# Kernel optimization log

Measured on AMD Instinct MI355X. Metric: run time of the kernel, lower is better.

## Reference

```python
import jax, jax.numpy as jnp
import numpy as np

B, T, IN, HID, BR, OUT = 128, 250, 700, 1024, 4, 20
VTH1, VTH2, DT = 0.5, 0.5, 1.0

# heaviside spike with multi-gaussian surrogate grad (DH-SNN ActFun_adp)
@jax.custom_vjp
def spike_fn(v):
    return (v > 0).astype(v.dtype)

def _spike_fwd(v):
    return spike_fn(v), v

def _spike_bwd(v, g):
    gamma, lens, scale, hight = 0.5, 0.5, 6.0, 0.15
    def gauss(x, mu, sigma):
        return jnp.exp(-((x - mu) ** 2) / (2.0 * sigma ** 2)) / (jnp.sqrt(2.0 * jnp.pi) * sigma)
    sg = (gauss(v, 0.0, lens) * (1.0 + hight)
          - gauss(v, lens, scale * lens) * hight
          - gauss(v, -lens, scale * lens) * hight)
    return (g * sg * gamma,)

spike_fn.defvjp(_spike_fwd, _spike_bwd)

def _make_mask(rng):
    # each output neuron's BR branches see disjoint equal slices of a random permutation
    K = IN + HID  # pad == 0 since (IN+HID) % BR == 0
    seg = K // BR
    mask = np.zeros((HID * BR, K), dtype=np.int32)
    for i in range(HID):
        seq = rng.permutation(K)
        for j in range(BR):
            mask[i * BR + j, seq[j * seg:(j + 1) * seg]] = 1
    return mask

def setup_inputs() -> dict:
    key = jax.random.key(0)
    ks = jax.random.split(key, 10)
    K = IN + HID
    x = jax.random.uniform(ks[0], (B, T, IN), dtype=jnp.float32)
    W1 = jax.random.normal(ks[1], (HID * BR, K), dtype=jnp.float32) / jnp.sqrt(jnp.float32(K))
    b1 = jnp.zeros((HID * BR,), jnp.float32)
    tau_m1 = jax.random.uniform(ks[2], (HID,), jnp.float32, 0.0, 4.0)
    tau_n = jax.random.uniform(ks[3], (HID, BR), jnp.float32, 0.0, 4.0)
    W2 = jax.random.normal(ks[4], (OUT, HID), dtype=jnp.float32) / jnp.sqrt(jnp.float32(HID))
    b2 = jnp.zeros((OUT,), jnp.float32)
    tau_m2 = jax.random.uniform(ks[5], (OUT,), jnp.float32, 0.0, 4.0)
    mem1_0 = jax.random.uniform(ks[6], (B, HID), jnp.float32)
    mem2_0 = jax.random.uniform(ks[7], (B, OUT), jnp.float32)
    mask = jnp.asarray(_make_mask(np.random.default_rng(0)))
    return dict(x=x, W1=W1, b1=b1, tau_m1=tau_m1, tau_n=tau_n, W2=W2, b2=b2,
                tau_m2=tau_m2, mem1_0=mem1_0, mem2_0=mem2_0, mask=mask)

def reference(x, W1, b1, tau_m1, tau_n, W2, b2, tau_m2, mem1_0, mem2_0, mask):
    bsz = x.shape[0]
    W1m = W1 * mask.astype(W1.dtype)  # branch-sparse dendritic weights
    alpha1 = jax.nn.sigmoid(tau_m1)   # [HID]
    beta = jax.nn.sigmoid(tau_n)      # [HID, BR]
    alpha2 = jax.nn.sigmoid(tau_m2)   # [OUT]
    spk1_0 = jnp.zeros((bsz, HID), x.dtype)
    d0 = jnp.zeros((bsz, HID, BR), x.dtype)
    spk2_0 = jnp.zeros((bsz, OUT), x.dtype)

    def step(carry, x_t):
        mem1, spk1, d_inp, mem2, spk2 = carry
        k_in = jnp.concatenate([x_t, spk1], axis=1)          # [B, IN+HID]
        ff = (k_in @ W1m.T + b1).reshape(bsz, HID, BR)       # dendritic branch input
        d_inp = beta * d_inp + (1.0 - beta) * ff             # per-branch decay
        l_in = d_inp.sum(axis=2)                             # [B, HID]
        mem1 = mem1 * alpha1 + (1.0 - alpha1) * l_in - VTH1 * spk1 * DT
        spk1 = spike_fn(mem1 - VTH1)
        d2 = spk1 @ W2.T + b2
        mem2 = mem2 * alpha2 + (1.0 - alpha2) * d2 - VTH2 * spk2 * DT
        spk2 = spike_fn(mem2 - VTH2)
        out = jax.nn.log_softmax(mem2, axis=1)
        return (mem1, spk1, d_inp, mem2, spk2), out

    _, ys = jax.lax.scan(step, (mem1_0, spk1_0, d0, mem2_0, spk2_0), jnp.swapaxes(x, 0, 1))
    return jnp.transpose(ys, (1, 2, 0))  # [B, OUT, T]
```

## Files before the change

### kernel.cpp

```cpp
#include <hip/hip_runtime.h>
#include <stdint.h>

#define BATCH 128
#define TSTEPS 250
#define NIN 700
#define NHID 1024
#define NBR 4
#define NOUT 20
#define KDIM 1724
#define NR 4096
#define VTH 0.5f

typedef float f32x4 __attribute__((ext_vector_type(4)));
typedef short s16x8 __attribute__((ext_vector_type(8)));


__global__ void setup_small(const float* __restrict__ tau_m1, const float* __restrict__ tau_n,
                            const float* __restrict__ tau_m2, const float* __restrict__ W2,
                            float* __restrict__ alpha1, float* __restrict__ beta,
                            float* __restrict__ alpha2, float* __restrict__ W2T) {
    int i = blockIdx.x * blockDim.x + threadIdx.x;
    if (i < NHID)  alpha1[i] = 1.f / (1.f + expf(-tau_m1[i]));
    if (i < NR)    beta[i]   = 1.f / (1.f + expf(-tau_n[i]));
    if (i < 32)    alpha2[i] = (i < NOUT) ? 1.f / (1.f + expf(-tau_m2[i])) : 0.f;
    if (i < NHID * 32) {
        int j = i >> 5, o = i & 31;
        W2T[i] = (o < NOUT) ? W2[o * NHID + j] : 0.f;
    }
}

__device__ __forceinline__ uint16_t f2bf_rne(float x) {
    uint32_t u = __float_as_uint(x);
    return (uint16_t)((u + 0x7FFFu + ((u >> 16) & 1u)) >> 16);
}

__global__ void setup_weights(const float* __restrict__ W1, const int* __restrict__ mask,
                              float* __restrict__ W1xT, uint16_t* __restrict__ fragH,
                              uint16_t* __restrict__ fragL) {
    const int total1 = NIN * NR;
    const int total2 = 256 * 16384;
    for (int i = blockIdx.x * blockDim.x + threadIdx.x; i < total1 + total2;
         i += gridDim.x * blockDim.x) {
        if (i < total1) {
            int k = i >> 12, r = i & 4095;
            size_t src = (size_t)r * KDIM + k;
            W1xT[i] = W1[src] * (float)mask[src];
        } else {
            int j2 = i - total1;
            int j = j2 & 7, lane = (j2 >> 3) & 63, ks = (j2 >> 9) & 31, blk = j2 >> 14;
            int k = ks * 32 + ((lane >> 4) & 3) * 8 + j;
            int r = blk * 16 + (lane & 15);
            size_t src = (size_t)r * KDIM + NIN + k;
            float w = W1[src] * (float)mask[src];
            uint16_t hb = f2bf_rne(w);
            float hf = __uint_as_float((uint32_t)hb << 16);
            fragH[j2] = hb;
            fragL[j2] = f2bf_rne(w - hf);
        }
    }
}

__global__ void init_state(const float* __restrict__ mem1_0, const float* __restrict__ mem2_0,
                           float* __restrict__ mem1, float* __restrict__ mem2,
                           float* __restrict__ spk2, float* __restrict__ d_inp,
                           uint32_t* __restrict__ spkg, uint32_t* __restrict__ bar) {
    int i = blockIdx.x * blockDim.x + threadIdx.x;
    if (i < BATCH * NR) d_inp[i] = 0.f;
    if (i < BATCH * NHID) mem1[i] = mem1_0[i];
    if (i < BATCH * NOUT) { mem2[i] = mem2_0[i]; spk2[i] = 0.f; }
    if (i < 8192) spkg[i] = 0u;
    if (i < 2048) bar[i] = 0u;
}


#define GBM 128
#define GBN 128
#define GBK 16

__global__ __launch_bounds__(256) void ffx_gemm(const float* __restrict__ x,
                                                const float* __restrict__ W1xT,
                                                const float* __restrict__ b1,
                                                float* __restrict__ ffx, int t0) {
    __shared__ float As[GBK][GBM];
    __shared__ float Bs[GBK][GBN];
    int dt = blockIdx.x, bn = blockIdx.y;
    int tid = threadIdx.x;
    int tn = tid & 15, tm = tid >> 4;

    float acc[8][8];
#pragma unroll
    for (int i = 0; i < 8; ++i)
#pragma unroll
        for (int j = 0; j < 8; ++j) acc[i][j] = 0.f;

    int m_l = tid >> 1;
    const float* xrow = x + ((size_t)m_l * TSTEPS + t0 + dt) * NIN;
    int kh = (tid & 1) * 8;
    int kb = tid >> 4;
    int nb = (tid & 15) * 8;

    for (int k0 = 0; k0 < NIN; k0 += GBK) {
        float av[8];
#pragma unroll
        for (int u = 0; u < 8; ++u) {
            int k = k0 + kh + u;
            av[u] = (k < NIN) ? xrow[k] : 0.f;
        }
#pragma unroll
        for (int u = 0; u < 8; ++u) As[kh + u][m_l] = av[u];

        bool kok = (k0 + kb) < NIN;
        const float* bp = W1xT + (size_t)(k0 + kb) * NR + bn * GBN + nb;
        float bv[8];
#pragma unroll
        for (int u = 0; u < 8; ++u) bv[u] = kok ? bp[u] : 0.f;
#pragma unroll
        for (int u = 0; u < 8; ++u) Bs[kb][nb + u] = bv[u];

        __syncthreads();
#pragma unroll
        for (int kk = 0; kk < GBK; ++kk) {
            float a[8], b[8];
#pragma unroll
            for (int u = 0; u < 8; ++u) a[u] = As[kk][tm * 8 + u];
#pragma unroll
            for (int u = 0; u < 8; ++u) b[u] = Bs[kk][tn * 8 + u];
#pragma unroll
            for (int i = 0; i < 8; ++i)
#pragma unroll
                for (int j = 0; j < 8; ++j) acc[i][j] += a[i] * b[j];
        }
        __syncthreads();
    }

    float bias[8];
#pragma unroll
    for (int j = 0; j < 8; ++j) bias[j] = b1[bn * GBN + tn * 8 + j];
#pragma unroll
    for (int i = 0; i < 8; ++i) {
        int brow = tm * 8 + i;
        float* cp = ffx + ((size_t)dt * BATCH + brow) * NR + bn * GBN + tn * 8;
#pragma unroll
        for (int j = 0; j < 8; ++j) cp[j] = acc[i][j] + bias[j];
    }
}


__global__ __launch_bounds__(1024) void persist6(
    const float* __restrict__ alpha1, const float* __restrict__ beta,
    const float* __restrict__ alpha2, float* __restrict__ mem1,
    float* __restrict__ mem2, float* __restrict__ spk2,
    float* __restrict__ d_inp, const uint16_t* __restrict__ fragH_g,
    const uint16_t* __restrict__ fragL_g, const float* __restrict__ W2T,
    const float* __restrict__ ffx, const float* __restrict__ b2v,
    float* __restrict__ out, uint32_t* __restrict__ spkg,
    uint32_t* __restrict__ bar, int t0, int tc, int last, int epoch0) {
    __shared__ __align__(16) uint16_t lds_fh[16384];
    __shared__ __align__(16) uint16_t lds_fl[16384];
    __shared__ uint32_t lds_spk[4096];
    __shared__ uint32_t lds_mask[128 * 33];
    __shared__ float lds_part[2560];
    __shared__ float lds_part2[2560];

    const int blk = blockIdx.x;
    const int tid = threadIdx.x;
    const int l   = tid & 63;
    const int wv  = tid >> 6;

    {
        const float4* sH = (const float4*)(fragH_g + (size_t)blk * 16384);
        const float4* sL = (const float4*)(fragL_g + (size_t)blk * 16384);
        for (int i4 = tid; i4 < 2048; i4 += 1024) {
            ((float4*)lds_fh)[i4] = sH[i4];
            ((float4*)lds_fl)[i4] = sL[i4];
        }
    }

    const int mt = wv & 7;
    const int kh = wv >> 3;
    const int arow = mt * 16 + (l & 15);
    const int ksl = ((l >> 4) & 3) * 8;

    const int ub    = tid >> 3;
    const int unrn  = (tid >> 1) & 3;
    const int uhalf = tid & 1;
    const int nrn_g = (blk << 2) + unrn;
    const int rl0   = unrn * 4 + uhalf * 2;
    const int r_g0  = (blk << 4) + rl0;
    const float bet0 = beta[r_g0];
    const float bet1 = beta[r_g0 + 1];
    const float al   = alpha1[nrn_g];
    float di0 = d_inp[(size_t)ub * NR + r_g0];
    float di1 = d_inp[(size_t)ub * NR + r_g0 + 1];
    float mm  = mem1[ub * NHID + nrn_g];

    const int o2 = tid & 31;
    const int sub = tid >> 5;
    const bool l2blk = (blk < 16) && ((sub & 3) == 0);
    const int b2b = (blk << 3) + (sub >> 2);
    float m2 = 0.f, s2v = 0.f, a2 = 0.f, bo = 0.f;
    if (l2blk && o2 < NOUT) {
        a2 = alpha2[o2];
        bo = b2v[o2];
        m2 = mem2[b2b * NOUT + o2];
        s2v = spk2[b2b * NOUT + o2];
    }

    const int grpid = blk & 15;
    uint32_t* grpcnt = &bar[32 * (1 + grpid)];
    uint32_t* goword = &bar[32 * (17 + grpid)];
    const bool leader = (blk >= 240);

    const int iters = tc + (last ? 1 : 0);
    for (int it = 0; it < iters; ++it) {
        const int tt = t0 + it;

        float ff0 = 0.f, ff1 = 0.f;
        if (tt < TSTEPS) {
            const float2 fv = *(const float2*)(ffx + (size_t)it * (BATCH * NR)
                                               + (size_t)ub * NR + r_g0);
            ff0 = fv.x; ff1 = fv.y;
        }

        if (it > 0) {
            if (tid == 0) {
                uint32_t tgt = (uint32_t)(epoch0 + it);
                if (leader) {
                    while (__hip_atomic_load(&bar[0], __ATOMIC_ACQUIRE,
                                             __HIP_MEMORY_SCOPE_AGENT) < 16u * tgt)
                        __builtin_amdgcn_s_sleep(2);
                    __hip_atomic_store(goword, tgt, __ATOMIC_RELEASE,
                                       __HIP_MEMORY_SCOPE_AGENT);
                } else {
                    while (__hip_atomic_load(goword, __ATOMIC_RELAXED,
                                             __HIP_MEMORY_SCOPE_AGENT) < tgt)
                        __builtin_amdgcn_s_sleep(2);
                }
            }
            __syncthreads();
        }

        {
            const uint32_t* spg = spkg + (size_t)((tt + 1) & 1) * 4096;
#pragma unroll
            for (int k = 0; k < 4; ++k) {
                int idx = tid + (k << 10);
                lds_spk[idx ^ ((idx >> 7) & 31)] =
                    __hip_atomic_load(&spg[idx], __ATOMIC_RELAXED, __HIP_MEMORY_SCOPE_AGENT);
            }
        }
        __syncthreads();

        {
            const int w = tid & 31;
            const int bq = tid >> 5;
            const int g = bq >> 1;
            uint32_t sw[8];
#pragma unroll
            for (int m = 0; m < 8; ++m) {
                int raw = (w << 7) + (m << 4) + g;
                sw[m] = lds_spk[raw ^ (w & 31)];
            }
#pragma unroll
            for (int u = 0; u < 4; ++u) {
                const int b = (bq << 2) + u;
                const int j = ((bq & 1) << 2) + u;
                uint32_t word = 0;
#pragma unroll
                for (int m = 0; m < 8; ++m)
                    word |= ((sw[m] >> (j << 2)) & 0xFu) << (m << 2);
                lds_mask[b * 33 + w] = word;
            }
        }
        __syncthreads();

        if (tt < TSTEPS) {
            f32x4 acc = {0.f, 0.f, 0.f, 0.f};
            const int maskbase = arow * 33;
#pragma unroll 4
            for (int i = 0; i < 16; ++i) {
                const int ks = kh * 16 + i;
                uint32_t bits = (lds_mask[maskbase + ks] >> ksl) & 0xFFu;
                union { uint32_t u[4]; s16x8 v; } a;
                a.u[0] = ((bits & 1u)  ? 0x3F80u : 0u) | ((bits & 2u)   ? 0x3F800000u : 0u);
                a.u[1] = ((bits & 4u)  ? 0x3F80u : 0u) | ((bits & 8u)   ? 0x3F800000u : 0u);
                a.u[2] = ((bits & 16u) ? 0x3F80u : 0u) | ((bits & 32u)  ? 0x3F800000u : 0u);
                a.u[3] = ((bits & 64u) ? 0x3F80u : 0u) | ((bits & 128u) ? 0x3F800000u : 0u);
                const s16x8 bh = *(const s16x8*)&lds_fh[(ks * 64 + l) * 8];
                const s16x8 bl = *(const s16x8*)&lds_fl[(ks * 64 + l) * 8];
                acc = __builtin_amdgcn_mfma_f32_16x16x32_bf16(a.v, bh, acc, 0, 0, 0);
                acc = __builtin_amdgcn_mfma_f32_16x16x32_bf16(a.v, bl, acc, 0, 0, 0);
            }
            float* pp = (kh == 0 ? lds_part : lds_part2)
                        + ((mt * 16 + (l & 15)) * 20 + ((l >> 4) & 3) * 4);
            *(float4*)pp = *(float4*)&acc;
        }
        __syncthreads();

        if (tt < TSTEPS) {
            const int pb = ((ub >> 4) * 16 + rl0) * 20 + (ub & 15);
            float s0 = lds_part[pb]      + lds_part2[pb];
            float s1 = lds_part[pb + 20] + lds_part2[pb + 20];
            di0 = bet0 * di0 + (1.f - bet0) * (s0 + ff0);
            di1 = bet1 * di1 + (1.f - bet1) * (s1 + ff1);
            float t2 = di0 + di1;
            float lsum = t2 + __shfl_xor(t2, 1);
            float sp_prev = (float)((lds_mask[ub * 33 + (nrn_g >> 5)] >> (nrn_g & 31)) & 1u);
            float mn = mm * al + (1.f - al) * lsum - VTH * sp_prev;
            mm = mn;
            bool spk = (mn - VTH) > 0.f;
            unsigned long long bal = __ballot(spk && (uhalf == 0));
            if (l == 0) {
                uint32_t dw = 0;
#pragma unroll
                for (int j = 0; j < 8; ++j) {
                    uint32_t v = (uint32_t)(bal >> (j * 8)) & 0x55u;
                    uint32_t nib = (v & 1u) | ((v >> 1) & 2u) | ((v >> 2) & 4u) | ((v >> 3) & 8u);
                    dw |= nib << (4 * j);
                }
                uint32_t* spn = spkg + (size_t)(tt & 1) * 4096;
                __hip_atomic_store(&spn[(blk << 4) + wv], dw, __ATOMIC_RELAXED,
                                   __HIP_MEMORY_SCOPE_AGENT);
            }
        }

        __syncthreads();
        if (it + 1 < iters && tid == 0) {
            uint32_t e16 = 16u * (uint32_t)(epoch0 + it + 1);
            uint32_t old = __hip_atomic_fetch_add(grpcnt, 1u, __ATOMIC_RELEASE,
                                                  __HIP_MEMORY_SCOPE_AGENT);
            if (old == e16 - 1u)
                __hip_atomic_fetch_add(&bar[0], 1u, __ATOMIC_RELEASE,
                                       __HIP_MEMORY_SCOPE_AGENT);
        }

        if (tt > 0 && l2blk) {
            const uint32_t* mw = &lds_mask[b2b * 33];
            float d2 = bo;
            for (int w = 0; w < 32; ++w) {
                uint32_t bits = mw[w];
                while (bits) {
                    int p = __builtin_ctz(bits);
                    bits &= bits - 1;
                    d2 += W2T[(((w << 5) + p) << 5) + o2];
                }
            }
            float m2n = m2 * a2 + (1.f - a2) * d2 - VTH * s2v;
            m2 = m2n;
            s2v = ((m2n - VTH) > 0.f) ? 1.f : 0.f;
            float v = (o2 < NOUT) ? m2n : -3.4e38f;
#pragma unroll
            for (int off = 16; off >= 1; off >>= 1) v = fmaxf(v, __shfl_xor(v, off, 32));
            float e = (o2 < NOUT) ? expf(m2n - v) : 0.f;
            float s = e;
#pragma unroll
            for (int off = 16; off >= 1; off >>= 1) s += __shfl_xor(s, off, 32);
            if (o2 < NOUT) out[((size_t)b2b * NOUT + o2) * TSTEPS + (tt - 1)] = (m2n - v) - logf(s);
        }
    }

    d_inp[(size_t)ub * NR + r_g0]     = di0;
    d_inp[(size_t)ub * NR + r_g0 + 1] = di1;
    if (uhalf == 0) mem1[ub * NHID + nrn_g] = mm;
    if (l2blk && o2 < NOUT) {
        mem2[b2b * NOUT + o2] = m2;
        spk2[b2b * NOUT + o2] = s2v;
    }
}


extern "C" void kernel_launch(void* const* d_in, const int* in_sizes, int n_in,
                              void* d_out, int out_size, void* d_ws, size_t ws_size,
                              hipStream_t stream) {
    const float* x      = (const float*)d_in[0];
    const float* W1     = (const float*)d_in[1];
    const float* b1     = (const float*)d_in[2];
    const float* tau_m1 = (const float*)d_in[3];
    const float* tau_n  = (const float*)d_in[4];
    const float* W2     = (const float*)d_in[5];
    const float* b2     = (const float*)d_in[6];
    const float* tau_m2 = (const float*)d_in[7];
    const float* mem1_0 = (const float*)d_in[8];
    const float* mem2_0 = (const float*)d_in[9];
    const int*   mask   = (const int*)d_in[10];
    float* out = (float*)d_out;

    float* ws = (float*)d_ws;
    size_t F = 0;
    float* alpha1 = ws + F; F += 1024;
    float* beta   = ws + F; F += 4096;
    float* alpha2 = ws + F; F += 32;
    float* mem1   = ws + F; F += BATCH * NHID;
    float* mem2   = ws + F; F += BATCH * NOUT;
    float* spk2   = ws + F; F += BATCH * NOUT;
    float* d_inp  = ws + F; F += BATCH * NR;
    float* W1xT   = ws + F; F += (size_t)NIN * NR;
    uint16_t* fragH = (uint16_t*)(ws + F); F += (size_t)256 * 16384 / 2;
    uint16_t* fragL = (uint16_t*)(ws + F); F += (size_t)256 * 16384 / 2;
    float* W2T    = ws + F; F += NHID * 32;
    uint32_t* spkg = (uint32_t*)(ws + F); F += 8192;
    uint32_t* bar  = (uint32_t*)(ws + F); F += 2048;
    float* ffx = ws + F;

    size_t ws_f = ws_size / 4;
    size_t avail = (ws_f > F) ? (ws_f - F) : 0;
    size_t per_t = (size_t)BATCH * NR;
    int Tc = (int)(avail / per_t);
    if (Tc < 1) Tc = 1;
    if (Tc > TSTEPS) Tc = TSTEPS;

    hipLaunchKernelGGL(setup_small, dim3(128), dim3(256), 0, stream,
                       tau_m1, tau_n, tau_m2, W2, alpha1, beta, alpha2, W2T);
    hipLaunchKernelGGL(setup_weights, dim3(2048), dim3(256), 0, stream,
                       W1, mask, W1xT, fragH, fragL);
    hipLaunchKernelGGL(init_state, dim3(2048), dim3(256), 0, stream,
                       mem1_0, mem2_0, mem1, mem2, spk2, d_inp, spkg, bar);

    int chunk_start = 0;
    int barriers_done = 0;
    while (chunk_start < TSTEPS) {
        int tc = TSTEPS - chunk_start;
        if (tc > Tc) tc = Tc;
        int last = (chunk_start + tc >= TSTEPS) ? 1 : 0;

        hipLaunchKernelGGL(ffx_gemm, dim3(tc, 32), dim3(256), 0, stream,
                           x, W1xT, b1, ffx, chunk_start);
        hipLaunchKernelGGL(persist6, dim3(256), dim3(1024), 0, stream,
                           alpha1, beta, alpha2, mem1, mem2, spk2, d_inp, fragH, fragL,
                           W2T, ffx, b2, out, spkg, bar, chunk_start, tc, last, barriers_done);

        int iters = tc + (last ? 1 : 0);
        barriers_done += iters - 1;
        chunk_start += tc;
    }
}
```

Measured before the change: 6.728 ms.

## Publish spikes in transposed global layout via atomic OR, drop LDS repack

Each timestep's spike bits are now written straight into a batch-major bitmask in global memory, using per-lane atomic OR into a 4-deep ring buffer, with a slot two steps ahead zeroed each step. Readers load their mask words directly from global, so the per-step LDS staging, the transpose/repack pass and two block-wide barriers go away. The cost is many small global atomics per step, and the correctness of the ring clearing depends on the grid barrier ordering.

```diff
diff --git a/kernel.cpp b/kernel.cpp
--- a/kernel.cpp
+++ b/kernel.cpp
@@ -63,12 +63,12 @@
 __global__ void init_state(const float* __restrict__ mem1_0, const float* __restrict__ mem2_0,
                            float* __restrict__ mem1, float* __restrict__ mem2,
                            float* __restrict__ spk2, float* __restrict__ d_inp,
-                           uint32_t* __restrict__ spkg, uint32_t* __restrict__ bar) {
+                           uint32_t* __restrict__ spkT, uint32_t* __restrict__ bar) {
     int i = blockIdx.x * blockDim.x + threadIdx.x;
     if (i < BATCH * NR) d_inp[i] = 0.f;
     if (i < BATCH * NHID) mem1[i] = mem1_0[i];
     if (i < BATCH * NOUT) { mem2[i] = mem2_0[i]; spk2[i] = 0.f; }
-    if (i < 8192) spkg[i] = 0u;
+    if (i < 4 * 4096) spkT[i] = 0u;
     if (i < 2048) bar[i] = 0u;
 }
 
@@ -146,19 +146,17 @@
 }
 
 
-__global__ __launch_bounds__(1024) void persist6(
+__global__ __launch_bounds__(1024) void persist8(
     const float* __restrict__ alpha1, const float* __restrict__ beta,
     const float* __restrict__ alpha2, float* __restrict__ mem1,
     float* __restrict__ mem2, float* __restrict__ spk2,
     float* __restrict__ d_inp, const uint16_t* __restrict__ fragH_g,
     const uint16_t* __restrict__ fragL_g, const float* __restrict__ W2T,
     const float* __restrict__ ffx, const float* __restrict__ b2v,
-    float* __restrict__ out, uint32_t* __restrict__ spkg,
+    float* __restrict__ out, uint32_t* __restrict__ spkT,
     uint32_t* __restrict__ bar, int t0, int tc, int last, int epoch0) {
     __shared__ __align__(16) uint16_t lds_fh[16384];
     __shared__ __align__(16) uint16_t lds_fl[16384];
-    __shared__ uint32_t lds_spk[4096];
-    __shared__ uint32_t lds_mask[128 * 33];
     __shared__ float lds_part[2560];
     __shared__ float lds_part2[2560];
 
@@ -240,47 +238,22 @@
             __syncthreads();
         }
 
-        {
-            const uint32_t* spg = spkg + (size_t)((tt + 1) & 1) * 4096;
-#pragma unroll
-            for (int k = 0; k < 4; ++k) {
-                int idx = tid + (k << 10);
-                lds_spk[idx ^ ((idx >> 7) & 31)] =
-                    __hip_atomic_load(&spg[idx], __ATOMIC_RELAXED, __HIP_MEMORY_SCOPE_AGENT);
-            }
-        }
-        __syncthreads();
-
-        {
-            const int w = tid & 31;
-            const int bq = tid >> 5;
-            const int g = bq >> 1;
-            uint32_t sw[8];
-#pragma unroll
-            for (int m = 0; m < 8; ++m) {
-                int raw = (w << 7) + (m << 4) + g;
-                sw[m] = lds_spk[raw ^ (w & 31)];
-            }
-#pragma unroll
-            for (int u = 0; u < 4; ++u) {
-                const int b = (bq << 2) + u;
-                const int j = ((bq & 1) << 2) + u;
-                uint32_t word = 0;
-#pragma unroll
-                for (int m = 0; m < 8; ++m)
-                    word |= ((sw[m] >> (j << 2)) & 0xFu) << (m << 2);
-                lds_mask[b * 33 + w] = word;
-            }
-        }
-        __syncthreads();
-
+        const uint32_t* spc = spkT + (size_t)(tt & 3) * 4096;
+
+        uint32_t spw = 0;
         if (tt < TSTEPS) {
+            spw = __hip_atomic_load(&spc[ub * 32 + (nrn_g >> 5)], __ATOMIC_RELAXED,
+                                    __HIP_MEMORY_SCOPE_AGENT);
+            uint32_t mw[16];
+#pragma unroll
+            for (int i = 0; i < 16; ++i)
+                mw[i] = __hip_atomic_load(&spc[arow * 32 + kh * 16 + i], __ATOMIC_RELAXED,
+                                          __HIP_MEMORY_SCOPE_AGENT);
             f32x4 acc = {0.f, 0.f, 0.f, 0.f};
-            const int maskbase = arow * 33;
 #pragma unroll 4
             for (int i = 0; i < 16; ++i) {
                 const int ks = kh * 16 + i;
-                uint32_t bits = (lds_mask[maskbase + ks] >> ksl) & 0xFFu;
+                uint32_t bits = (mw[i] >> ksl) & 0xFFu;
                 union { uint32_t u[4]; s16x8 v; } a;
                 a.u[0] = ((bits & 1u)  ? 0x3F80u : 0u) | ((bits & 2u)   ? 0x3F800000u : 0u);
                 a.u[1] = ((bits & 4u)  ? 0x3F80u : 0u) | ((bits & 8u)   ? 0x3F800000u : 0u);
@@ -305,23 +278,25 @@
             di1 = bet1 * di1 + (1.f - bet1) * (s1 + ff1);
             float t2 = di0 + di1;
             float lsum = t2 + __shfl_xor(t2, 1);
-            float sp_prev = (float)((lds_mask[ub * 33 + (nrn_g >> 5)] >> (nrn_g & 31)) & 1u);
+            float sp_prev = (float)((spw >> (nrn_g & 31)) & 1u);
             float mn = mm * al + (1.f - al) * lsum - VTH * sp_prev;
             mm = mn;
             bool spk = (mn - VTH) > 0.f;
             unsigned long long bal = __ballot(spk && (uhalf == 0));
-            if (l == 0) {
-                uint32_t dw = 0;
-#pragma unroll
-                for (int j = 0; j < 8; ++j) {
-                    uint32_t v = (uint32_t)(bal >> (j * 8)) & 0x55u;
-                    uint32_t nib = (v & 1u) | ((v >> 1) & 2u) | ((v >> 2) & 4u) | ((v >> 3) & 8u);
-                    dw |= nib << (4 * j);
-                }
-                uint32_t* spn = spkg + (size_t)(tt & 1) * 4096;
-                __hip_atomic_store(&spn[(blk << 4) + wv], dw, __ATOMIC_RELAXED,
-                                   __HIP_MEMORY_SCOPE_AGENT);
+            if ((l & 7) == 0) {
+                int b = (wv << 3) + (l >> 3);
+                uint32_t v = (uint32_t)(bal >> l) & 0x55u;
+                uint32_t nib = (v & 1u) | ((v >> 1) & 2u) | ((v >> 2) & 4u) | ((v >> 3) & 8u);
+                uint32_t* spn = spkT + (size_t)((tt + 1) & 3) * 4096;
+                __hip_atomic_fetch_or(&spn[b * 32 + (blk >> 3)], nib << ((blk & 7) * 4),
+                                      __ATOMIC_RELAXED, __HIP_MEMORY_SCOPE_AGENT);
             }
+        }
+
+        if (tt < TSTEPS && tid < 16) {
+            uint32_t* spz = spkT + (size_t)((tt + 2) & 3) * 4096;
+            __hip_atomic_store(&spz[(blk << 4) + tid], 0u, __ATOMIC_RELAXED,
+                               __HIP_MEMORY_SCOPE_AGENT);
         }
 
         __syncthreads();
@@ -335,10 +310,11 @@
         }
 
         if (tt > 0 && l2blk) {
-            const uint32_t* mw = &lds_mask[b2b * 33];
             float d2 = bo;
+#pragma unroll
             for (int w = 0; w < 32; ++w) {
-                uint32_t bits = mw[w];
+                uint32_t bits = __hip_atomic_load(&spc[b2b * 32 + w], __ATOMIC_RELAXED,
+                                                  __HIP_MEMORY_SCOPE_AGENT);
                 while (bits) {
                     int p = __builtin_ctz(bits);
                     bits &= bits - 1;
@@ -398,7 +374,7 @@
     uint16_t* fragH = (uint16_t*)(ws + F); F += (size_t)256 * 16384 / 2;
     uint16_t* fragL = (uint16_t*)(ws + F); F += (size_t)256 * 16384 / 2;
     float* W2T    = ws + F; F += NHID * 32;
-    uint32_t* spkg = (uint32_t*)(ws + F); F += 8192;
+    uint32_t* spkT = (uint32_t*)(ws + F); F += 4 * 4096;
     uint32_t* bar  = (uint32_t*)(ws + F); F += 2048;
     float* ffx = ws + F;
 
@@ -414,7 +390,7 @@
     hipLaunchKernelGGL(setup_weights, dim3(2048), dim3(256), 0, stream,
                        W1, mask, W1xT, fragH, fragL);
     hipLaunchKernelGGL(init_state, dim3(2048), dim3(256), 0, stream,
-                       mem1_0, mem2_0, mem1, mem2, spk2, d_inp, spkg, bar);
+                       mem1_0, mem2_0, mem1, mem2, spk2, d_inp, spkT, bar);
 
     int chunk_start = 0;
     int barriers_done = 0;
@@ -425,9 +401,9 @@
 
         hipLaunchKernelGGL(ffx_gemm, dim3(tc, 32), dim3(256), 0, stream,
                            x, W1xT, b1, ffx, chunk_start);
-        hipLaunchKernelGGL(persist6, dim3(256), dim3(1024), 0, stream,
+        hipLaunchKernelGGL(persist8, dim3(256), dim3(1024), 0, stream,
                            alpha1, beta, alpha2, mem1, mem2, spk2, d_inp, fragH, fragL,
-                           W2T, ffx, b2, out, spkg, bar, chunk_start, tc, last, barriers_done);
+                           W2T, ffx, b2, out, spkT, bar, chunk_start, tc, last, barriers_done);
 
         int iters = tc + (last ? 1 : 0);
         barriers_done += iters - 1;
```

Result: slower. 8.349 ms (+24.1%).

## Split persistent recurrence into two independent batch-half groups with separate barriers

Applied to the files above, without the earlier changes.

The persistent kernel now splits the batch into two halves of 64, each served by its own group of 128 blocks of 512 threads. Each block owns 32 rows of the recurrent weights instead of 16, and uses independent hi/lo MFMA accumulators rather than a K-split. Each half synchronises only its own 128 blocks through a separate barrier region and spike buffer. The aim is cheaper grid barriers with fewer participants and less spike data gathered per step, at the cost of twice the LDS weight footprint per block and fewer threads per block.

```diff
diff --git a/kernel.cpp b/kernel.cpp
--- a/kernel.cpp
+++ b/kernel.cpp
@@ -38,7 +38,7 @@
                               float* __restrict__ W1xT, uint16_t* __restrict__ fragH,
                               uint16_t* __restrict__ fragL) {
     const int total1 = NIN * NR;
-    const int total2 = 256 * 16384;
+    const int total2 = 128 << 15;
     for (int i = blockIdx.x * blockDim.x + threadIdx.x; i < total1 + total2;
          i += gridDim.x * blockDim.x) {
         if (i < total1) {
@@ -46,16 +46,17 @@
             size_t src = (size_t)r * KDIM + k;
             W1xT[i] = W1[src] * (float)mask[src];
         } else {
-            int j2 = i - total1;
-            int j = j2 & 7, lane = (j2 >> 3) & 63, ks = (j2 >> 9) & 31, blk = j2 >> 14;
+            int e = i - total1;
+            int j = e & 7, lane = (e >> 3) & 63, ks = (e >> 9) & 31;
+            int nt2 = (e >> 14) & 1, gb = e >> 15;
             int k = ks * 32 + ((lane >> 4) & 3) * 8 + j;
-            int r = blk * 16 + (lane & 15);
+            int r = gb * 32 + nt2 * 16 + (lane & 15);
             size_t src = (size_t)r * KDIM + NIN + k;
             float w = W1[src] * (float)mask[src];
             uint16_t hb = f2bf_rne(w);
             float hf = __uint_as_float((uint32_t)hb << 16);
-            fragH[j2] = hb;
-            fragL[j2] = f2bf_rne(w - hf);
+            fragH[e] = hb;
+            fragL[e] = f2bf_rne(w - hf);
         }
     }
 }
@@ -146,7 +147,7 @@
 }
 
 
-__global__ __launch_bounds__(1024) void persist6(
+__global__ __launch_bounds__(512) void persist9(
     const float* __restrict__ alpha1, const float* __restrict__ beta,
     const float* __restrict__ alpha2, float* __restrict__ mem1,
     float* __restrict__ mem2, float* __restrict__ spk2,
@@ -155,84 +156,81 @@
     const float* __restrict__ ffx, const float* __restrict__ b2v,
     float* __restrict__ out, uint32_t* __restrict__ spkg,
     uint32_t* __restrict__ bar, int t0, int tc, int last, int epoch0) {
-    __shared__ __align__(16) uint16_t lds_fh[16384];
-    __shared__ __align__(16) uint16_t lds_fl[16384];
-    __shared__ uint32_t lds_spk[4096];
-    __shared__ uint32_t lds_mask[128 * 33];
+    __shared__ __align__(16) uint16_t lds_fh[32768];
+    __shared__ __align__(16) uint16_t lds_fl[32768];
+    __shared__ uint32_t lds_raw[2048];
+    __shared__ uint32_t lds_mask[64 * 33];
     __shared__ float lds_part[2560];
-    __shared__ float lds_part2[2560];
 
     const int blk = blockIdx.x;
     const int tid = threadIdx.x;
+    const int G   = blk >> 7;
+    const int gb  = blk & 127;
     const int l   = tid & 63;
     const int wv  = tid >> 6;
 
     {
-        const float4* sH = (const float4*)(fragH_g + (size_t)blk * 16384);
-        const float4* sL = (const float4*)(fragL_g + (size_t)blk * 16384);
-        for (int i4 = tid; i4 < 2048; i4 += 1024) {
+        const float4* sH = (const float4*)(fragH_g + (size_t)gb * 32768);
+        const float4* sL = (const float4*)(fragL_g + (size_t)gb * 32768);
+        for (int i4 = tid; i4 < 4096; i4 += 512) {
             ((float4*)lds_fh)[i4] = sH[i4];
             ((float4*)lds_fl)[i4] = sL[i4];
         }
     }
 
-    const int mt = wv & 7;
-    const int kh = wv >> 3;
+    const int mt  = wv >> 1;
+    const int nt2 = wv & 1;
     const int arow = mt * 16 + (l & 15);
-    const int ksl = ((l >> 4) & 3) * 8;
-
-    const int ub    = tid >> 3;
-    const int unrn  = (tid >> 1) & 3;
-    const int uhalf = tid & 1;
-    const int nrn_g = (blk << 2) + unrn;
-    const int rl0   = unrn * 4 + uhalf * 2;
-    const int r_g0  = (blk << 4) + rl0;
-    const float bet0 = beta[r_g0];
-    const float bet1 = beta[r_g0 + 1];
-    const float al   = alpha1[nrn_g];
-    float di0 = d_inp[(size_t)ub * NR + r_g0];
-    float di1 = d_inp[(size_t)ub * NR + r_g0 + 1];
-    float mm  = mem1[ub * NHID + nrn_g];
+    const int ksl  = ((l >> 4) & 3) * 8;
+
+    const int ub = tid >> 3;
+    const int un = tid & 7;
+    const int bg_ = G * 64 + ub;
+    const int n_g = gb * 8 + un;
+    const int r0  = gb * 32 + un * 4;
+    const f32x4 bet = *(const f32x4*)&beta[r0];
+    const float al  = alpha1[n_g];
+    f32x4 di = *(const f32x4*)&d_inp[(size_t)bg_ * NR + r0];
+    float mm = mem1[bg_ * NHID + n_g];
 
     const int o2 = tid & 31;
     const int sub = tid >> 5;
-    const bool l2blk = (blk < 16) && ((sub & 3) == 0);
-    const int b2b = (blk << 3) + (sub >> 2);
+    const bool l2blk = (gb < 16) && ((sub & 3) == 0);
+    const int b2l = gb * 4 + (sub >> 2);
+    const int b2g = G * 64 + b2l;
     float m2 = 0.f, s2v = 0.f, a2 = 0.f, bo = 0.f;
     if (l2blk && o2 < NOUT) {
         a2 = alpha2[o2];
         bo = b2v[o2];
-        m2 = mem2[b2b * NOUT + o2];
-        s2v = spk2[b2b * NOUT + o2];
-    }
-
-    const int grpid = blk & 15;
-    uint32_t* grpcnt = &bar[32 * (1 + grpid)];
-    uint32_t* goword = &bar[32 * (17 + grpid)];
-    const bool leader = (blk >= 240);
+        m2 = mem2[b2g * NOUT + o2];
+        s2v = spk2[b2g * NOUT + o2];
+    }
+
+    uint32_t* breg = bar + (size_t)G * 1024;
+    const int sg = gb & 7;
+    uint32_t* grpcnt = &breg[32 * (1 + sg)];
+    uint32_t* goline = &breg[32 * (9 + sg)];
+    const bool leader = (gb >= 120);
 
     const int iters = tc + (last ? 1 : 0);
     for (int it = 0; it < iters; ++it) {
         const int tt = t0 + it;
 
-        float ff0 = 0.f, ff1 = 0.f;
-        if (tt < TSTEPS) {
-            const float2 fv = *(const float2*)(ffx + (size_t)it * (BATCH * NR)
-                                               + (size_t)ub * NR + r_g0);
-            ff0 = fv.x; ff1 = fv.y;
-        }
+        f32x4 ff = {0.f, 0.f, 0.f, 0.f};
+        if (tt < TSTEPS)
+            ff = *(const f32x4*)(ffx + (size_t)it * (BATCH * NR) + (size_t)bg_ * NR + r0);
 
         if (it > 0) {
             if (tid == 0) {
                 uint32_t tgt = (uint32_t)(epoch0 + it);
                 if (leader) {
-                    while (__hip_atomic_load(&bar[0], __ATOMIC_ACQUIRE,
-                                             __HIP_MEMORY_SCOPE_AGENT) < 16u * tgt)
+                    while (__hip_atomic_load(&breg[0], __ATOMIC_ACQUIRE,
+                                             __HIP_MEMORY_SCOPE_AGENT) < 8u * tgt)
                         __builtin_amdgcn_s_sleep(2);
-                    __hip_atomic_store(goword, tgt, __ATOMIC_RELEASE,
+                    __hip_atomic_store(goline, tgt, __ATOMIC_RELEASE,
                                        __HIP_MEMORY_SCOPE_AGENT);
                 } else {
-                    while (__hip_atomic_load(goword, __ATOMIC_RELAXED,
+                    while (__hip_atomic_load(goline, __ATOMIC_RELAXED,
                                              __HIP_MEMORY_SCOPE_AGENT) < tgt)
                         __builtin_amdgcn_s_sleep(2);
                 }
@@ -241,87 +239,81 @@
         }
 
         {
-            const uint32_t* spg = spkg + (size_t)((tt + 1) & 1) * 4096;
-#pragma unroll
-            for (int k = 0; k < 4; ++k) {
-                int idx = tid + (k << 10);
-                lds_spk[idx ^ ((idx >> 7) & 31)] =
+            const uint32_t* spg = spkg + (size_t)((tt + 1) & 1) * 4096 + G * 2048;
+#pragma unroll
+            for (int k2 = 0; k2 < 4; ++k2) {
+                int idx = tid + (k2 << 9);
+                lds_raw[idx ^ ((idx >> 6) & 31)] =
                     __hip_atomic_load(&spg[idx], __ATOMIC_RELAXED, __HIP_MEMORY_SCOPE_AGENT);
             }
         }
         __syncthreads();
 
         {
-            const int w = tid & 31;
-            const int bq = tid >> 5;
-            const int g = bq >> 1;
-            uint32_t sw[8];
-#pragma unroll
-            for (int m = 0; m < 8; ++m) {
-                int raw = (w << 7) + (m << 4) + g;
-                sw[m] = lds_spk[raw ^ (w & 31)];
-            }
-#pragma unroll
-            for (int u = 0; u < 4; ++u) {
-                const int b = (bq << 2) + u;
-                const int j = ((bq & 1) << 2) + u;
+#pragma unroll
+            for (int k2 = 0; k2 < 4; ++k2) {
+                int e = tid + (k2 << 9);
+                int b = e >> 5, w = e & 31;
                 uint32_t word = 0;
 #pragma unroll
-                for (int m = 0; m < 8; ++m)
-                    word |= ((sw[m] >> (j << 2)) & 0xFu) << (m << 2);
+                for (int m = 0; m < 4; ++m) {
+                    int raw = ((w << 2) + m) * 16 + (b >> 2);
+                    uint32_t v = lds_raw[raw ^ ((raw >> 6) & 31)];
+                    word |= ((v >> ((b & 3) * 8)) & 0xFFu) << (m * 8);
+                }
                 lds_mask[b * 33 + w] = word;
             }
         }
         __syncthreads();
 
         if (tt < TSTEPS) {
-            f32x4 acc = {0.f, 0.f, 0.f, 0.f};
+            f32x4 accH = {0.f, 0.f, 0.f, 0.f};
+            f32x4 accL = {0.f, 0.f, 0.f, 0.f};
             const int maskbase = arow * 33;
+            const int fbase = nt2 * 32;
 #pragma unroll 4
-            for (int i = 0; i < 16; ++i) {
-                const int ks = kh * 16 + i;
+            for (int ks = 0; ks < 32; ++ks) {
                 uint32_t bits = (lds_mask[maskbase + ks] >> ksl) & 0xFFu;
                 union { uint32_t u[4]; s16x8 v; } a;
                 a.u[0] = ((bits & 1u)  ? 0x3F80u : 0u) | ((bits & 2u)   ? 0x3F800000u : 0u);
                 a.u[1] = ((bits & 4u)  ? 0x3F80u : 0u) | ((bits & 8u)   ? 0x3F800000u : 0u);
                 a.u[2] = ((bits & 16u) ? 0x3F80u : 0u) | ((bits & 32u)  ? 0x3F800000u : 0u);
                 a.u[3] = ((bits & 64u) ? 0x3F80u : 0u) | ((bits & 128u) ? 0x3F800000u : 0u);
-                const s16x8 bh = *(const s16x8*)&lds_fh[(ks * 64 + l) * 8];
-                const s16x8 bl = *(const s16x8*)&lds_fl[(ks * 64 + l) * 8];
-                acc = __builtin_amdgcn_mfma_f32_16x16x32_bf16(a.v, bh, acc, 0, 0, 0);
-                acc = __builtin_amdgcn_mfma_f32_16x16x32_bf16(a.v, bl, acc, 0, 0, 0);
+                const s16x8 bh = *(const s16x8*)&lds_fh[((fbase + ks) * 64 + l) * 8];
+                const s16x8 bl = *(const s16x8*)&lds_fl[((fbase + ks) * 64 + l) * 8];
+                accH = __builtin_amdgcn_mfma_f32_16x16x32_bf16(a.v, bh, accH, 0, 0, 0);
+                accL = __builtin_amdgcn_mfma_f32_16x16x32_bf16(a.v, bl, accL, 0, 0, 0);
             }
-            float* pp = (kh == 0 ? lds_part : lds_part2)
-                        + ((mt * 16 + (l & 15)) * 20 + ((l >> 4) & 3) * 4);
-            *(float4*)pp = *(float4*)&acc;
+            f32x4 d;
+#pragma unroll
+            for (int q = 0; q < 4; ++q) d[q] = accH[q] + accL[q];
+            float* pp = lds_part + ((mt * 32 + nt2 * 16 + (l & 15)) * 20 + ((l >> 4) & 3) * 4);
+            *(float4*)pp = *(float4*)&d;
         }
         __syncthreads();
 
         if (tt < TSTEPS) {
-            const int pb = ((ub >> 4) * 16 + rl0) * 20 + (ub & 15);
-            float s0 = lds_part[pb]      + lds_part2[pb];
-            float s1 = lds_part[pb + 20] + lds_part2[pb + 20];
-            di0 = bet0 * di0 + (1.f - bet0) * (s0 + ff0);
-            di1 = bet1 * di1 + (1.f - bet1) * (s1 + ff1);
-            float t2 = di0 + di1;
-            float lsum = t2 + __shfl_xor(t2, 1);
-            float sp_prev = (float)((lds_mask[ub * 33 + (nrn_g >> 5)] >> (nrn_g & 31)) & 1u);
+            const int rl0 = un * 4;
+            float s[4];
+#pragma unroll
+            for (int q = 0; q < 4; ++q)
+                s[q] = lds_part[((ub >> 4) * 32 + rl0 + q) * 20 + (ub & 15)];
+#pragma unroll
+            for (int q = 0; q < 4; ++q)
+                di[q] = bet[q] * di[q] + (1.f - bet[q]) * (s[q] + ff[q]);
+            float lsum = (di[0] + di[1]) + (di[2] + di[3]);
+            float sp_prev = (float)((lds_mask[ub * 33 + (n_g >> 5)] >> (n_g & 31)) & 1u);
             float mn = mm * al + (1.f - al) * lsum - VTH * sp_prev;
             mm = mn;
             bool spk = (mn - VTH) > 0.f;
-            unsigned long long bal = __ballot(spk && (uhalf == 0));
-            if (l == 0) {
-                uint32_t dw = 0;
-#pragma unroll
-                for (int j = 0; j < 8; ++j) {
-                    uint32_t v = (uint32_t)(bal >> (j * 8)) & 0x55u;
-                    uint32_t nib = (v & 1u) | ((v >> 1) & 2u) | ((v >> 2) & 4u) | ((v >> 3) & 8u);
-                    dw |= nib << (4 * j);
-                }
-                uint32_t* spn = spkg + (size_t)(tt & 1) * 4096;
-                __hip_atomic_store(&spn[(blk << 4) + wv], dw, __ATOMIC_RELAXED,
-                                   __HIP_MEMORY_SCOPE_AGENT);
-            }
+            unsigned long long bal = __ballot(spk);
+            uint32_t* spn = spkg + (size_t)(tt & 1) * 4096 + G * 2048;
+            if (l == 0)
+                __hip_atomic_store(&spn[gb * 16 + wv * 2], (uint32_t)bal,
+                                   __ATOMIC_RELAXED, __HIP_MEMORY_SCOPE_AGENT);
+            if (l == 32)
+                __hip_atomic_store(&spn[gb * 16 + wv * 2 + 1], (uint32_t)(bal >> 32),
+                                   __ATOMIC_RELAXED, __HIP_MEMORY_SCOPE_AGENT);
         }
 
         __syncthreads();
@@ -330,12 +322,12 @@
             uint32_t old = __hip_atomic_fetch_add(grpcnt, 1u, __ATOMIC_RELEASE,
                                                   __HIP_MEMORY_SCOPE_AGENT);
             if (old == e16 - 1u)
-                __hip_atomic_fetch_add(&bar[0], 1u, __ATOMIC_RELEASE,
+                __hip_atomic_fetch_add(&breg[0], 1u, __ATOMIC_RELEASE,
                                        __HIP_MEMORY_SCOPE_AGENT);
         }
 
         if (tt > 0 && l2blk) {
-            const uint32_t* mw = &lds_mask[b2b * 33];
+            const uint32_t* mw = &lds_mask[b2l * 33];
             float d2 = bo;
             for (int w = 0; w < 32; ++w) {
                 uint32_t bits = mw[w];
@@ -352,19 +344,18 @@
 #pragma unroll
             for (int off = 16; off >= 1; off >>= 1) v = fmaxf(v, __shfl_xor(v, off, 32));
             float e = (o2 < NOUT) ? expf(m2n - v) : 0.f;
-            float s = e;
-#pragma unroll
-            for (int off = 16; off >= 1; off >>= 1) s += __shfl_xor(s, off, 32);
-            if (o2 < NOUT) out[((size_t)b2b * NOUT + o2) * TSTEPS + (tt - 1)] = (m2n - v) - logf(s);
-        }
-    }
-
-    d_inp[(size_t)ub * NR + r_g0]     = di0;
-    d_inp[(size_t)ub * NR + r_g0 + 1] = di1;
-    if (uhalf == 0) mem1[ub * NHID + nrn_g] = mm;
+            float ssum = e;
+#pragma unroll
+            for (int off = 16; off >= 1; off >>= 1) ssum += __shfl_xor(ssum, off, 32);
+            if (o2 < NOUT) out[((size_t)b2g * NOUT + o2) * TSTEPS + (tt - 1)] = (m2n - v) - logf(ssum);
+        }
+    }
+
+    *(f32x4*)&d_inp[(size_t)bg_ * NR + r0] = di;
+    mem1[bg_ * NHID + n_g] = mm;
     if (l2blk && o2 < NOUT) {
-        mem2[b2b * NOUT + o2] = m2;
-        spk2[b2b * NOUT + o2] = s2v;
+        mem2[b2g * NOUT + o2] = m2;
+        spk2[b2g * NOUT + o2] = s2v;
     }
 }
 
@@ -395,8 +386,8 @@
     float* spk2   = ws + F; F += BATCH * NOUT;
     float* d_inp  = ws + F; F += BATCH * NR;
     float* W1xT   = ws + F; F += (size_t)NIN * NR;
-    uint16_t* fragH = (uint16_t*)(ws + F); F += (size_t)256 * 16384 / 2;
-    uint16_t* fragL = (uint16_t*)(ws + F); F += (size_t)256 * 16384 / 2;
+    uint16_t* fragH = (uint16_t*)(ws + F); F += (size_t)(128 << 15) / 2;
+    uint16_t* fragL = (uint16_t*)(ws + F); F += (size_t)(128 << 15) / 2;
     float* W2T    = ws + F; F += NHID * 32;
     uint32_t* spkg = (uint32_t*)(ws + F); F += 8192;
     uint32_t* bar  = (uint32_t*)(ws + F); F += 2048;
@@ -425,7 +416,7 @@
 
         hipLaunchKernelGGL(ffx_gemm, dim3(tc, 32), dim3(256), 0, stream,
                            x, W1xT, b1, ffx, chunk_start);
-        hipLaunchKernelGGL(persist6, dim3(256), dim3(1024), 0, stream,
+        hipLaunchKernelGGL(persist9, dim3(256), dim3(512), 0, stream,
                            alpha1, beta, alpha2, mem1, mem2, spk2, d_inp, fragH, fragL,
                            W2T, ffx, b2, out, spkg, bar, chunk_start, tc, last, barriers_done);
 
```

Result: faster. 6.111 ms, median of 2 (-9.2%).
